# Kernel tuning notes

Measured on AMD Instinct MI355X. Metric: run time of the kernel, lower is better.

The kernel has to match this reference:

```python
import jax, jax.numpy as jnp
import numpy as np

DIAG_PENALTY = 100.0

def setup_inputs() -> dict:
    key = jax.random.key(0)
    x = jax.random.normal(key, (8192, 768), dtype=jnp.float32)
    return {"x": x, "coef": 1.0, "tau": 1.0}

def _similarity(x):
    # sim[i, j] = -||x_i - x_j||^2, computed via GEMM expansion
    # ||a - b||^2 = ||a||^2 + ||b||^2 - 2 a.b  (avoids the (N,N,D) intermediate)
    sq = jnp.sum(x * x, axis=1)                      # [N]
    gram = x @ x.T                                   # [N, N]
    sim = 2.0 * gram - sq[:, None] - sq[None, :]     # = -||x_i - x_j||^2
    n = x.shape[0]
    sim = sim - DIAG_PENALTY * jnp.eye(n, dtype=x.dtype)
    return sim

def reference(x, coef, tau):
    sim = _similarity(x) * tau                       # [N, N]
    logp = jax.nn.log_softmax(sim, axis=-1)          # stable, single pass
    prob = jnp.exp(logp)
    entropy = -jnp.sum(prob * logp, axis=-1)         # [N]
    return coef * jnp.mean(entropy)
```

## Files before the change

kernel.cpp:

```cpp
#include <hip/hip_runtime.h>
#include <hip/hip_bf16.h>
#include <hip/hip_fp8.h>
#include <cstdint>
#include <cstddef>

#define GN 8192
#define GD 768
#define NB 64
#define NTILE 2080
#define KI 12

#define LOG2E 1.4426950408889634f
#define LN2 0.6931471805599453f

typedef __attribute__((ext_vector_type(4))) float f32x4;
typedef __attribute__((ext_vector_type(16))) float f32x16;
typedef __attribute__((ext_vector_type(4))) int i32x4;
typedef __attribute__((ext_vector_type(8))) int i32x8;

typedef __attribute__((address_space(1))) const unsigned int gu32;
typedef __attribute__((address_space(3))) unsigned int lu32;

#define SHUF8(L, H) __builtin_shufflevector(L, H, 0, 1, 2, 3, 4, 5, 6, 7)
#define Z16 {0.f, 0.f, 0.f, 0.f, 0.f, 0.f, 0.f, 0.f, 0.f, 0.f, 0.f, 0.f, 0.f, 0.f, 0.f, 0.f}
#define MXFMA(A, B, C) __builtin_amdgcn_mfma_scale_f32_32x32x64_f8f6f4( \
    A, B, C, 0, 0, 0, 0x7f7f7f7f, 0, 0x7f7f7f7f)

__device__ __forceinline__ void gl2lds16(const void* g, void* l) {
    __builtin_amdgcn_global_load_lds((gu32*)g, (lu32*)l, 16, 0, 0);
}

__device__ __forceinline__ float hexp2(float x) {
    return __builtin_amdgcn_exp2f(x);
}

template <int CTRL>
__device__ __forceinline__ float fdpp(float x) {
    return __int_as_float(__builtin_amdgcn_update_dpp(
        0, __float_as_int(x), CTRL, 0xF, 0xF, true));
}
__device__ __forceinline__ float qmax16(float v) {
    v = fmaxf(v, fdpp<0x128>(v));
    v = fmaxf(v, fdpp<0x124>(v));
    v = fmaxf(v, fdpp<0x122>(v));
    v = fmaxf(v, fdpp<0x121>(v));
    return v;
}
__device__ __forceinline__ float qsum16(float v) {
    v += fdpp<0x128>(v);
    v += fdpp<0x124>(v);
    v += fdpp<0x122>(v);
    v += fdpp<0x121>(v);
    return v;
}

__device__ __forceinline__ int swz(int r, int q) {
    return ((r >> 1) << 7) + (((((r & 1) << 2) | q) ^ ((r >> 1) & 7)) << 4);
}

__global__ __launch_bounds__(256) void prep_kernel(const float* __restrict__ x,
                                                   unsigned char* __restrict__ xq,
                                                   float* __restrict__ sq,
                                                   float* __restrict__ out) {
    if (blockIdx.x == 0 && threadIdx.x == 0) out[0] = 0.f;
    const int w = threadIdx.x >> 6, lane = threadIdx.x & 63;
    const int row = blockIdx.x * 4 + w;
    const float4* xr = (const float4*)(x + (size_t)row * GD);
    unsigned int* xqr = (unsigned int*)(xq + (size_t)row * GD);
    float s = 0.f;
#pragma unroll
    for (int i = 0; i < 3; ++i) {
        float4 v = xr[lane + 64 * i];
        unsigned int pk = __builtin_amdgcn_cvt_pk_fp8_f32(v.x, v.y, 0, false);
        pk = __builtin_amdgcn_cvt_pk_fp8_f32(v.z, v.w, pk, true);
        float d0 = __builtin_amdgcn_cvt_f32_fp8(pk, 0);
        float d1 = __builtin_amdgcn_cvt_f32_fp8(pk, 1);
        float d2 = __builtin_amdgcn_cvt_f32_fp8(pk, 2);
        float d3 = __builtin_amdgcn_cvt_f32_fp8(pk, 3);
        s += d0 * d0 + d1 * d1 + d2 * d2 + d3 * d3;
        xqr[lane + 64 * i] = pk;
    }
#pragma unroll
    for (int off = 1; off < 64; off <<= 1) s += __shfl_xor(s, off);
    if (lane == 0) sq[row] = s;
}

__global__ __launch_bounds__(256, 3) void sym_gemm_entropy(
    const unsigned char* __restrict__ xq, const float* __restrict__ sq,
    const float* __restrict__ taup, float* __restrict__ pm,
    float* __restrict__ ps, float* __restrict__ pt) {
    __shared__ __align__(16) char lds[32768];
    float (*tmrg)[4][3] = (float (*)[4][3])lds;

    const int tid = threadIdx.x;
    const int lane = tid & 63;
    const int w = tid >> 6;
    const int cl2 = lane & 31, hi = lane >> 5;

    const int b = blockIdx.x;
    int I = (int)((sqrtf(8.0f * (float)b + 1.0f) - 1.0f) * 0.5f);
    while ((I + 1) * (I + 2) / 2 <= b) ++I;
    while (I * (I + 1) / 2 > b) --I;
    const int J = b - I * (I + 1) / 2;
    const int row_base = I * 128;
    const int col_base = J * 128;
    const float taub = (*taup) * LOG2E;

    const int bb = (tid & 7) ^ ((tid >> 3) & 7);
    const int sRow = ((tid >> 3) << 1) | (bb >> 2);
    const int sKb = (bb & 3) * 16;
    const unsigned char* gA = xq + (size_t)(row_base + sRow) * GD + sKb;
    const unsigned char* gB = xq + (size_t)(col_base + sRow) * GD + sKb;

    const int offA0 = swz(w * 32 + cl2, 2 * hi);
    const int offA1 = swz(w * 32 + cl2, 2 * hi + 1);
    const int offB00 = swz(0 * 32 + cl2, 2 * hi), offB01 = swz(0 * 32 + cl2, 2 * hi + 1);
    const int offB10 = swz(1 * 32 + cl2, 2 * hi), offB11 = swz(1 * 32 + cl2, 2 * hi + 1);
    const int offB20 = swz(2 * 32 + cl2, 2 * hi), offB21 = swz(2 * 32 + cl2, 2 * hi + 1);
    const int offB30 = swz(3 * 32 + cl2, 2 * hi), offB31 = swz(3 * 32 + cl2, 2 * hi + 1);

    f32x16 acc0 = Z16, acc1 = Z16, acc2 = Z16, acc3 = Z16;

    gl2lds16(gA, lds + tid * 16);
    gl2lds16(gA + (size_t)64 * GD, lds + 4096 + tid * 16);
    gl2lds16(gB, lds + 8192 + tid * 16);
    gl2lds16(gB + (size_t)64 * GD, lds + 12288 + tid * 16);

#pragma unroll 2
    for (int kk = 0; kk < KI; ++kk) {
        __syncthreads();

        const char* Ab = lds + (kk & 1) * 16384;
        const char* Bb = Ab + 8192;
        i32x4 aL = *(const i32x4*)(Ab + offA0);
        i32x4 aH = *(const i32x4*)(Ab + offA1);
        i32x4 b0L = *(const i32x4*)(Bb + offB00), b0H = *(const i32x4*)(Bb + offB01);
        i32x4 b1L = *(const i32x4*)(Bb + offB10), b1H = *(const i32x4*)(Bb + offB11);
        i32x4 b2L = *(const i32x4*)(Bb + offB20), b2H = *(const i32x4*)(Bb + offB21);
        i32x4 b3L = *(const i32x4*)(Bb + offB30), b3H = *(const i32x4*)(Bb + offB31);
        i32x8 av = SHUF8(aL, aH);
        i32x8 bv0 = SHUF8(b0L, b0H), bv1 = SHUF8(b1L, b1H);
        i32x8 bv2 = SHUF8(b2L, b2H), bv3 = SHUF8(b3L, b3H);

        if (kk + 1 < KI) {
            char* An = lds + ((kk + 1) & 1) * 16384;
            const int ko = (kk + 1) * 64;
            gl2lds16(gA + ko, An + tid * 16);
            gl2lds16(gA + (size_t)64 * GD + ko, An + 4096 + tid * 16);
            gl2lds16(gB + ko, An + 8192 + tid * 16);
            gl2lds16(gB + (size_t)64 * GD + ko, An + 12288 + tid * 16);
        }

        acc0 = MXFMA(av, bv0, acc0);
        acc1 = MXFMA(av, bv1, acc1);
        acc2 = MXFMA(av, bv2, acc2);
        acc3 = MXFMA(av, bv3, acc3);
    }

    f32x4 pa[4][4];
#define SPLIT16(TJ, A)                                          \
    pa[TJ][0] = __builtin_shufflevector(A, A, 0, 1, 2, 3);      \
    pa[TJ][1] = __builtin_shufflevector(A, A, 4, 5, 6, 7);      \
    pa[TJ][2] = __builtin_shufflevector(A, A, 8, 9, 10, 11);    \
    pa[TJ][3] = __builtin_shufflevector(A, A, 12, 13, 14, 15);
    SPLIT16(0, acc0)
    SPLIT16(1, acc1)
    SPLIT16(2, acc2)
    SPLIT16(3, acc3)
#undef SPLIT16

    const float t2 = 2.f * taub;
    const float pen = 100.f * taub;
    float ar[16];
#pragma unroll
    for (int q = 0; q < 4; ++q)
#pragma unroll
        for (int rg = 0; rg < 4; ++rg)
            ar[q * 4 + rg] = -taub * sq[row_base + w * 32 + rg + 8 * q + 4 * hi];
    float ac[4];
#pragma unroll
    for (int tj = 0; tj < 4; ++tj) ac[tj] = -taub * sq[col_base + tj * 32 + cl2];

    float* pmJ = pm + (size_t)J * GN;
    float* psJ = ps + (size_t)J * GN;
    float* ptJ = pt + (size_t)J * GN;

#pragma unroll
    for (int q = 0; q < 4; ++q)
#pragma unroll
        for (int rg = 0; rg < 4; ++rg) {
            const int rl = rg + 8 * q + 4 * hi;
            const int rglob = row_base + w * 32 + rl;
            float uu[4];
            float mloc = -1e30f;
            if (I == J) {
#pragma unroll
                for (int tj = 0; tj < 4; ++tj) {
                    float u = fmaf(t2, pa[tj][q][rg], ac[tj]);
                    if (rglob == col_base + tj * 32 + cl2) u -= pen;
                    uu[tj] = u;
                    mloc = fmaxf(mloc, u);
                }
            } else {
#pragma unroll
                for (int tj = 0; tj < 4; ++tj) {
                    float u = fmaf(t2, pa[tj][q][rg], ac[tj]);
                    uu[tj] = u;
                    mloc = fmaxf(mloc, u);
                }
            }
            mloc = fmaxf(mloc, __shfl_xor(mloc, 16));
            mloc = qmax16(mloc);
            float s = 0.f, t = 0.f;
#pragma unroll
            for (int tj = 0; tj < 4; ++tj) {
                float d = uu[tj] - mloc;
                float e = hexp2(d);
                s += e;
                t += e * d;
            }
            s += __shfl_xor(s, 16);
            t += __shfl_xor(t, 16);
            s = qsum16(s);
            t = qsum16(t);
            if (cl2 == 0) {
                pmJ[rglob] = mloc + ar[q * 4 + rg];
                psJ[rglob] = s;
                ptJ[rglob] = t;
            }
        }

    if (I != J) {
        __syncthreads();
#pragma unroll
        for (int tj = 0; tj < 4; ++tj) {
            float uu[16];
            float mloc = -1e30f;
#pragma unroll
            for (int q = 0; q < 4; ++q)
#pragma unroll
                for (int rg = 0; rg < 4; ++rg) {
                    float u = fmaf(t2, pa[tj][q][rg], ar[q * 4 + rg]);
                    uu[q * 4 + rg] = u;
                    mloc = fmaxf(mloc, u);
                }
            mloc = fmaxf(mloc, __shfl_xor(mloc, 32));
            float s = 0.f, t = 0.f;
#pragma unroll
            for (int k = 0; k < 16; ++k) {
                float d = uu[k] - mloc;
                float e = hexp2(d);
                s += e;
                t += e * d;
            }
            s += __shfl_xor(s, 32);
            t += __shfl_xor(t, 32);
            if (hi == 0) {
                int c = tj * 32 + cl2;
                tmrg[c][w][0] = mloc + ac[tj];
                tmrg[c][w][1] = s;
                tmrg[c][w][2] = t;
            }
        }
        __syncthreads();
        if (tid < 128) {
            float m = tmrg[tid][0][0], S = tmrg[tid][0][1], T = tmrg[tid][0][2];
#pragma unroll
            for (int ww = 1; ww < 4; ++ww) {
                float mc = tmrg[tid][ww][0], Sc = tmrg[tid][ww][1], Tc = tmrg[tid][ww][2];
                float mn = fmaxf(m, mc);
                float ea = hexp2(m - mn), eb = hexp2(mc - mn);
                T = (T + (m - mn) * S) * ea + (Tc + (mc - mn) * Sc) * eb;
                S = S * ea + Sc * eb;
                m = mn;
            }
            int c = col_base + tid;
            pm[(size_t)I * GN + c] = m;
            ps[(size_t)I * GN + c] = S;
            pt[(size_t)I * GN + c] = T;
        }
    }
}

__global__ __launch_bounds__(256) void combine(const float* __restrict__ pm,
                                               const float* __restrict__ ps,
                                               const float* __restrict__ pt,
                                               const float* __restrict__ coefp,
                                               float* __restrict__ out) {
    const int t = threadIdx.x;
    const int r = t & 63;
    const int chunk = t >> 6;
    const int row = blockIdx.x * 64 + r;
    float m = -1e30f, S = 0.f, T = 0.f;
#pragma unroll
    for (int i = 0; i < 16; ++i) {
        const int c = chunk * 16 + i;
        float mc = pm[(size_t)c * GN + row];
        float Sc = ps[(size_t)c * GN + row];
        float Tc = pt[(size_t)c * GN + row];
        float mn = fmaxf(m, mc);
        float ea = __builtin_amdgcn_exp2f(m - mn), eb = __builtin_amdgcn_exp2f(mc - mn);
        T = (T + (m - mn) * S) * ea + (Tc + (mc - mn) * Sc) * eb;
        S = S * ea + Sc * eb;
        m = mn;
    }
    __shared__ float lm[4][64], lS[4][64], lT[4][64];
    lm[chunk][r] = m;
    lS[chunk][r] = S;
    lT[chunk][r] = T;
    __syncthreads();
    if (t < 64) {
        float M = lm[0][r], Sa = lS[0][r], Ta = lT[0][r];
#pragma unroll
        for (int cc = 1; cc < 4; ++cc) {
            float mc = lm[cc][r], Sc = lS[cc][r], Tc = lT[cc][r];
            float mn = fmaxf(M, mc);
            float ea = __builtin_amdgcn_exp2f(M - mn), eb = __builtin_amdgcn_exp2f(mc - mn);
            Ta = (Ta + (M - mn) * Sa) * ea + (Tc + (mc - mn) * Sc) * eb;
            Sa = Sa * ea + Sc * eb;
            M = mn;
        }
        float ent2 = __log2f(Sa) - Ta / Sa;
#pragma unroll
        for (int off = 1; off < 64; off <<= 1) ent2 += __shfl_xor(ent2, off);
        if (t == 0) atomicAdd(out, ent2 * coefp[0] * (LN2 / (float)GN));
    }
}

extern "C" void kernel_launch(void* const* d_in, const int* in_sizes, int n_in,
                              void* d_out, int out_size, void* d_ws, size_t ws_size,
                              hipStream_t stream) {
    const float* x = (const float*)d_in[0];
    const float* coefp = (const float*)d_in[1];
    const float* taup = (const float*)d_in[2];
    float* out = (float*)d_out;

    char* ws = (char*)d_ws;
    unsigned char* xq = (unsigned char*)ws;
    float* sq = (float*)(ws + 6291456);
    float* pm = (float*)(ws + 6324224);
    float* ps = (float*)(ws + 6324224 + 2097152);
    float* pt = (float*)(ws + 6324224 + 2 * 2097152);

    prep_kernel<<<GN / 4, 256, 0, stream>>>(x, xq, sq, out);
    sym_gemm_entropy<<<NTILE, 256, 0, stream>>>(xq, sq, taup, pm, ps, pt);
    combine<<<GN / 64, 256, 0, stream>>>(pm, ps, pt, coefp, out);
}
```

Before: 132.5 us.

## Load A operand directly from global into registers, stage only B in LDS

After: 149.1 us. 1.13x slower.

```diff
diff --git a/kernel.cpp b/kernel.cpp
--- a/kernel.cpp
+++ b/kernel.cpp
@@ -52,10 +52,6 @@
     v += fdpp<0x122>(v);
     v += fdpp<0x121>(v);
     return v;
-}
-
-__device__ __forceinline__ int swz(int r, int q) {
-    return ((r >> 1) << 7) + (((((r & 1) << 2) | q) ^ ((r >> 1) & 7)) << 4);
 }
 
 __global__ __launch_bounds__(256) void prep_kernel(const float* __restrict__ x,
@@ -89,7 +85,7 @@
     const unsigned char* __restrict__ xq, const float* __restrict__ sq,
     const float* __restrict__ taup, float* __restrict__ pm,
     float* __restrict__ ps, float* __restrict__ pt) {
-    __shared__ __align__(16) char lds[32768];
+    __shared__ __align__(16) char lds[16384];
     float (*tmrg)[4][3] = (float (*)[4][3])lds;
 
     const int tid = threadIdx.x;
@@ -106,55 +102,63 @@
     const int col_base = J * 128;
     const float taub = (*taup) * LOG2E;
 
-    const int bb = (tid & 7) ^ ((tid >> 3) & 7);
-    const int sRow = ((tid >> 3) << 1) | (bb >> 2);
-    const int sKb = (bb & 3) * 16;
-    const unsigned char* gA = xq + (size_t)(row_base + sRow) * GD + sKb;
-    const unsigned char* gB = xq + (size_t)(col_base + sRow) * GD + sKb;
-
-    const int offA0 = swz(w * 32 + cl2, 2 * hi);
-    const int offA1 = swz(w * 32 + cl2, 2 * hi + 1);
-    const int offB00 = swz(0 * 32 + cl2, 2 * hi), offB01 = swz(0 * 32 + cl2, 2 * hi + 1);
-    const int offB10 = swz(1 * 32 + cl2, 2 * hi), offB11 = swz(1 * 32 + cl2, 2 * hi + 1);
-    const int offB20 = swz(2 * 32 + cl2, 2 * hi), offB21 = swz(2 * 32 + cl2, 2 * hi + 1);
-    const int offB30 = swz(3 * 32 + cl2, 2 * hi), offB31 = swz(3 * 32 + cl2, 2 * hi + 1);
+    {
+    }
+    const int sS = tid & 127;
+    const int ggS = tid >> 7;
+    const int qloS = (sS >> 6) & 1, qhiS = (sS >> 5) & 1;
+    const int r4S = (sS >> 4) & 1, r3S = (sS >> 3) & 1;
+    const int rlowS = (sS & 7) ^ ((qhiS << 1) | r4S);
+    const int rB = ggS * 32 + ((r4S << 4) | (r3S << 3) | rlowS);
+    const int qB = (qhiS << 1) | qloS;
+    const unsigned char* gB = xq + (size_t)(col_base + rB) * GD + qB * 16;
+
+    const int r4L = (cl2 >> 4) & 1, r3L = (cl2 >> 3) & 1;
+    const int bsl = (cl2 & 7) ^ ((hi << 1) | r4L);
+    const int s0 = (hi << 5) | (r4L << 4) | (r3L << 3) | bsl;
+    const int offB00 = 0 * 2048 + (s0 << 4), offB01 = offB00 + 1024;
+    const int offB10 = 1 * 2048 + (s0 << 4), offB11 = offB10 + 1024;
+    const int offB20 = 2 * 2048 + (s0 << 4), offB21 = offB20 + 1024;
+    const int offB30 = 3 * 2048 + (s0 << 4), offB31 = offB30 + 1024;
+
+    const unsigned char* gAr =
+        xq + (size_t)(row_base + w * 32 + cl2) * GD + 32 * hi;
 
     f32x16 acc0 = Z16, acc1 = Z16, acc2 = Z16, acc3 = Z16;
 
-    gl2lds16(gA, lds + tid * 16);
-    gl2lds16(gA + (size_t)64 * GD, lds + 4096 + tid * 16);
-    gl2lds16(gB, lds + 8192 + tid * 16);
-    gl2lds16(gB + (size_t)64 * GD, lds + 12288 + tid * 16);
+    gl2lds16(gB, lds + tid * 16);
+    gl2lds16(gB + (size_t)64 * GD, lds + 4096 + tid * 16);
+    i32x4 aCL = *(const i32x4*)(gAr);
+    i32x4 aCH = *(const i32x4*)(gAr + 16);
+    i32x4 aNL = aCL, aNH = aCH;
 
 #pragma unroll 2
     for (int kk = 0; kk < KI; ++kk) {
         __syncthreads();
 
-        const char* Ab = lds + (kk & 1) * 16384;
-        const char* Bb = Ab + 8192;
-        i32x4 aL = *(const i32x4*)(Ab + offA0);
-        i32x4 aH = *(const i32x4*)(Ab + offA1);
+        const char* Bb = lds + (kk & 1) * 8192;
         i32x4 b0L = *(const i32x4*)(Bb + offB00), b0H = *(const i32x4*)(Bb + offB01);
         i32x4 b1L = *(const i32x4*)(Bb + offB10), b1H = *(const i32x4*)(Bb + offB11);
         i32x4 b2L = *(const i32x4*)(Bb + offB20), b2H = *(const i32x4*)(Bb + offB21);
         i32x4 b3L = *(const i32x4*)(Bb + offB30), b3H = *(const i32x4*)(Bb + offB31);
-        i32x8 av = SHUF8(aL, aH);
-        i32x8 bv0 = SHUF8(b0L, b0H), bv1 = SHUF8(b1L, b1H);
-        i32x8 bv2 = SHUF8(b2L, b2H), bv3 = SHUF8(b3L, b3H);
 
         if (kk + 1 < KI) {
-            char* An = lds + ((kk + 1) & 1) * 16384;
+            char* Bn = lds + ((kk + 1) & 1) * 8192;
             const int ko = (kk + 1) * 64;
-            gl2lds16(gA + ko, An + tid * 16);
-            gl2lds16(gA + (size_t)64 * GD + ko, An + 4096 + tid * 16);
-            gl2lds16(gB + ko, An + 8192 + tid * 16);
-            gl2lds16(gB + (size_t)64 * GD + ko, An + 12288 + tid * 16);
-        }
-
-        acc0 = MXFMA(av, bv0, acc0);
-        acc1 = MXFMA(av, bv1, acc1);
-        acc2 = MXFMA(av, bv2, acc2);
-        acc3 = MXFMA(av, bv3, acc3);
+            gl2lds16(gB + ko, Bn + tid * 16);
+            gl2lds16(gB + (size_t)64 * GD + ko, Bn + 4096 + tid * 16);
+            aNL = *(const i32x4*)(gAr + ko);
+            aNH = *(const i32x4*)(gAr + ko + 16);
+        }
+
+        i32x8 av = SHUF8(aCL, aCH);
+        acc0 = MXFMA(av, SHUF8(b0L, b0H), acc0);
+        acc1 = MXFMA(av, SHUF8(b1L, b1H), acc1);
+        acc2 = MXFMA(av, SHUF8(b2L, b2H), acc2);
+        acc3 = MXFMA(av, SHUF8(b3L, b3H), acc3);
+
+        aCL = aNL;
+        aCH = aNH;
     }
 
     f32x4 pa[4][4];
```
